# Kernel tuning notes

Measured on AMD Instinct MI355X. Metric: run time of the kernel, lower is better.

The kernel has to match this reference:

```python
import jax, jax.numpy as jnp
import numpy as np

HEADS = 4
OUT_CH = 64
NEG_SLOPE = 0.2  # PyG GATConv default negative_slope


def setup_inputs() -> dict:
    key = jax.random.key(0)
    k1, k2, k3, k4, k5, k6 = jax.random.split(key, 6)
    N, E, IN_CH = 50000, 800000, 128
    x = jax.random.normal(k1, (N, IN_CH), dtype=jnp.float32)
    edge_index = jax.random.randint(k2, (2, E), 0, N, dtype=jnp.int64)
    # Learned parameters (glorot-style init)
    s_w = (6.0 / (IN_CH + HEADS * OUT_CH)) ** 0.5
    W = jax.random.uniform(k3, (IN_CH, HEADS * OUT_CH), minval=-s_w, maxval=s_w, dtype=jnp.float32)
    s_a = (6.0 / (1 + OUT_CH)) ** 0.5
    att_src = jax.random.uniform(k4, (HEADS, OUT_CH), minval=-s_a, maxval=s_a, dtype=jnp.float32)
    att_dst = jax.random.uniform(k5, (HEADS, OUT_CH), minval=-s_a, maxval=s_a, dtype=jnp.float32)
    bias = jnp.zeros((HEADS * OUT_CH,), dtype=jnp.float32)
    return {"x": x, "W": W, "att_src": att_src, "att_dst": att_dst, "bias": bias, "edge_index": edge_index}


def reference(x, W, att_src, att_dst, bias, edge_index):
    # Faithful GATConv (PyG defaults: add_self_loops=True, concat=True, eval mode => no dropout)
    N = x.shape[0]
    loops = jnp.arange(N, dtype=edge_index.dtype)
    src = jnp.concatenate([edge_index[0], loops])  # message source j
    dst = jnp.concatenate([edge_index[1], loops])  # message target i

    xp = (x @ W).reshape(N, HEADS, OUT_CH)          # [N, H, C]
    a_src = jnp.einsum('nhc,hc->nh', xp, att_src)   # [N, H]
    a_dst = jnp.einsum('nhc,hc->nh', xp, att_dst)   # [N, H]

    alpha = jax.nn.leaky_relu(a_src[src] + a_dst[dst], NEG_SLOPE)  # [E', H]
    # segment softmax over incoming edges of each target node
    amax = jax.ops.segment_max(alpha, dst, num_segments=N)
    ex = jnp.exp(alpha - jax.lax.stop_gradient(amax)[dst])
    denom = jax.ops.segment_sum(ex, dst, num_segments=N)
    coef = ex / denom[dst]                           # [E', H]

    msg = xp[src] * coef[:, :, None]                 # [E', H, C]
    out = jax.ops.segment_sum(msg, dst, num_segments=N)  # [N, H, C]
    return out.reshape(N, HEADS * OUT_CH) + bias
```

## Files before the change

### kernel.cpp

```cpp
#include <hip/hip_runtime.h>

#define HEADS 4
#define OUTC 64
#define INC 128
#define HC 256
#define NEG 0.2f

typedef __attribute__((ext_vector_type(8))) short bf16x8;
typedef __attribute__((ext_vector_type(4))) float f32x4;

static __device__ __forceinline__ float bf2f(unsigned short u){
  unsigned int x = ((unsigned int)u) << 16;
  return __uint_as_float(x);
}
static __device__ __forceinline__ unsigned short f2bf(float f){
  unsigned int x = __float_as_uint(f);
  unsigned int lsb = (x >> 16) & 1u;
  x += 0x7fffu + lsb;
  return (unsigned short)(x >> 16);
}
static __device__ __forceinline__ void split8(float4 a, float4 b, bf16x8& hi, bf16x8& lo){
  float v[8] = {a.x, a.y, a.z, a.w, b.x, b.y, b.z, b.w};
  #pragma unroll
  for (int i = 0; i < 8; ++i){
    unsigned short h = f2bf(v[i]);
    hi[i] = (short)h;
    lo[i] = (short)f2bf(v[i] - bf2f(h));
  }
}

#define SPLITB 128

__global__ void k_pre(const float* __restrict__ W, unsigned short* __restrict__ Wthi,
                      unsigned short* __restrict__ Wtlo, const int* __restrict__ ei,
                      int* __restrict__ srcc, int* __restrict__ dstc,
                      int* __restrict__ pos, int* __restrict__ deg, int E){
  if (blockIdx.x < SPLITB){
    int t = blockIdx.x * 256 + threadIdx.x;
    int k = t >> 8, n = t & 255;
    float v = W[t];
    unsigned short hi = f2bf(v);
    Wthi[n * INC + k] = hi;
    Wtlo[n * INC + k] = f2bf(v - bf2f(hi));
    return;
  }
  int e = (blockIdx.x - SPLITB) * 256 + threadIdx.x;
  bool valid = (e < E);
  int ee = valid ? e : 0;
  int hiw = ei[2 * ee + 1];
  bool hz = valid ? (hiw == 0) : true;
  unsigned long long mask = __ballot(hz);
  bool i64 = (mask == ~0ULL);
  int s, d;
  if (i64){ s = ei[2 * ee]; d = ei[2 * (size_t)E + 2 * ee]; }
  else    { s = ei[ee];     d = ei[(size_t)E + ee]; }
  if (valid){
    srcc[e] = s; dstc[e] = d;
    pos[e] = atomicAdd(&deg[d], 1);
  }
}

__global__ __launch_bounds__(256) void k_gemm_scan(const float* __restrict__ X,
    const unsigned short* __restrict__ Wthi, const unsigned short* __restrict__ Wtlo,
    const float* __restrict__ att_src, const float* __restrict__ att_dst,
    unsigned short* __restrict__ XPh, float* __restrict__ a_src, float* __restrict__ a_dst,
    const int* __restrict__ deg, int* __restrict__ rowstart, int* __restrict__ bsum,
    int N, int GB, int nb){
  __shared__ unsigned short shi[64][40];
  __shared__ unsigned short slo[64][40];
  __shared__ int tsum[256];

  if (blockIdx.x >= GB){
    int sb = blockIdx.x - GB;
    int t = threadIdx.x;
    int base = sb * 1024 + t * 4;
    int v[4]; int s = 0;
    #pragma unroll
    for (int k = 0; k < 4; ++k){ int i = base + k; v[k] = (i < N) ? deg[i] : 0; s += v[k]; }
    tsum[t] = s;
    __syncthreads();
    for (int off = 1; off < 256; off <<= 1){
      int x = (t >= off) ? tsum[t - off] : 0;
      __syncthreads();
      tsum[t] += x;
      __syncthreads();
    }
    int excl = tsum[t] - s;
    if (t == 255){
      bsum[sb] = tsum[255];
      if (sb == nb - 1) rowstart[N] = tsum[255];
    }
    int run = excl;
    #pragma unroll
    for (int k = 0; k < 4; ++k){ int i = base + k; if (i < N) rowstart[i] = run; run += v[k]; }
    return;
  }

  int w = threadIdx.x >> 6, lane = threadIdx.x & 63;
  int m0 = blockIdx.x * 64;
  int quad = lane >> 4;
  int l15 = lane & 15;
  int colg[4];
  #pragma unroll
  for (int t = 0; t < 4; ++t) colg[t] = w * 64 + t * 16 + l15;

  bool rv[4];
  #pragma unroll
  for (int rt = 0; rt < 4; ++rt) rv[rt] = (m0 + rt * 16) < N;
  int myrow = rv[w] ? (m0 + w * 16 + l15) : 0;

  f32x4 acc[4][4];
  #pragma unroll
  for (int rt = 0; rt < 4; ++rt)
    #pragma unroll
    for (int t = 0; t < 4; ++t) acc[rt][t] = (f32x4){0.f, 0.f, 0.f, 0.f};

  #pragma unroll
  for (int kk = 0; kk < 4; ++kk){
    const float* xr = X + (size_t)myrow * INC + kk * 32 + quad * 8;
    float4 va = *(const float4*)xr;
    float4 vb = *(const float4*)(xr + 4);
    bf16x8 bh[4], bl[4];
    #pragma unroll
    for (int t = 0; t < 4; ++t){
      size_t bo = (size_t)colg[t] * INC + kk * 32 + quad * 8;
      bh[t] = *(const bf16x8*)(Wthi + bo);
      bl[t] = *(const bf16x8*)(Wtlo + bo);
    }
    bf16x8 ah1, al1;
    split8(va, vb, ah1, al1);
    if (kk) __syncthreads();
    *(bf16x8*)&shi[w * 16 + l15][quad * 8] = ah1;
    *(bf16x8*)&slo[w * 16 + l15][quad * 8] = al1;
    __syncthreads();
    bf16x8 ah[4], al[4];
    #pragma unroll
    for (int rt = 0; rt < 4; ++rt){
      ah[rt] = *(const bf16x8*)&shi[rt * 16 + l15][quad * 8];
      al[rt] = *(const bf16x8*)&slo[rt * 16 + l15][quad * 8];
    }
    #pragma unroll
    for (int rt = 0; rt < 4; ++rt){
      #pragma unroll
      for (int t = 0; t < 4; ++t){
        acc[rt][t] = __builtin_amdgcn_mfma_f32_16x16x32_bf16(ah[rt], bh[t], acc[rt][t], 0, 0, 0);
        acc[rt][t] = __builtin_amdgcn_mfma_f32_16x16x32_bf16(ah[rt], bl[t], acc[rt][t], 0, 0, 0);
        acc[rt][t] = __builtin_amdgcn_mfma_f32_16x16x32_bf16(al[rt], bh[t], acc[rt][t], 0, 0, 0);
      }
    }
  }

  #pragma unroll
  for (int rt = 0; rt < 4; ++rt){
    if (!rv[rt]) continue;
    #pragma unroll
    for (int t = 0; t < 4; ++t){
      #pragma unroll
      for (int r = 0; r < 4; ++r){
        XPh[(size_t)(m0 + rt * 16 + quad * 4 + r) * HC + colg[t]] = f2bf(acc[rt][t][r]);
      }
    }
  }

  float as[4], ad[4];
  #pragma unroll
  for (int t = 0; t < 4; ++t){
    as[t] = att_src[colg[t]];
    ad[t] = att_dst[colg[t]];
  }
  #pragma unroll
  for (int rt = 0; rt < 4; ++rt){
    if (!rv[rt]) continue;
    float ps[4], pd[4];
    #pragma unroll
    for (int r = 0; r < 4; ++r){
      ps[r] = acc[rt][0][r] * as[0] + acc[rt][1][r] * as[1]
            + acc[rt][2][r] * as[2] + acc[rt][3][r] * as[3];
      pd[r] = acc[rt][0][r] * ad[0] + acc[rt][1][r] * ad[1]
            + acc[rt][2][r] * ad[2] + acc[rt][3][r] * ad[3];
    }
    #pragma unroll
    for (int msk = 1; msk < 16; msk <<= 1){
      #pragma unroll
      for (int r = 0; r < 4; ++r){
        ps[r] += __shfl_xor(ps[r], msk, 64);
        pd[r] += __shfl_xor(pd[r], msk, 64);
      }
    }
    if (l15 == 0){
      #pragma unroll
      for (int r = 0; r < 4; ++r){
        int n = m0 + rt * 16 + quad * 4 + r;
        a_src[n * HEADS + w] = ps[r];
        a_dst[n * HEADS + w] = pd[r];
      }
    }
  }
}

__global__ __launch_bounds__(256) void k_scatter(const int* __restrict__ srcc,
                          const int* __restrict__ dstc, const int* __restrict__ pos,
                          const int* __restrict__ rowstart, const int* __restrict__ bsum,
                          int* __restrict__ csr, int E, int nb){
  __shared__ int bps[65];
  int t = threadIdx.x;
  if (t < 64){
    int v = (t < nb) ? bsum[t] : 0;
    #pragma unroll
    for (int off = 1; off < 64; off <<= 1){
      int u = __shfl_up(v, off, 64);
      if (t >= off) v += u;
    }
    bps[t + 1] = v;
    if (t == 0) bps[0] = 0;
  }
  __syncthreads();
  int e = blockIdx.x * 256 + t;
  if (e < E){
    int d = dstc[e];
    csr[rowstart[d] + bps[d >> 10] + pos[e]] = srcc[e];
  }
}

__global__ __launch_bounds__(256) void k_fused(const unsigned short* __restrict__ XPh,
    const float* __restrict__ a_src, const float* __restrict__ a_dst,
    const int* __restrict__ rowstart, const int* __restrict__ bsum,
    const int* __restrict__ csr, const float* __restrict__ bias,
    float* __restrict__ out, int n0, int n1, int nb){
  __shared__ float sh[4][64][4];
  __shared__ int bps[65];
  int w = threadIdx.x >> 6, lane = threadIdx.x & 63;
  if (threadIdx.x < 64){
    int v = (threadIdx.x < nb) ? bsum[threadIdx.x] : 0;
    #pragma unroll
    for (int off = 1; off < 64; off <<= 1){
      int u = __shfl_up(v, off, 64);
      if (threadIdx.x >= off) v += u;
    }
    bps[threadIdx.x + 1] = v;
    if (threadIdx.x == 0) bps[0] = 0;
  }
  __syncthreads();

  int n = n0 + blockIdx.x * 4 + w;
  bool alive = (n < n1);
  if (!alive) n = n0;
  int r0 = rowstart[n] + bps[n >> 10];
  int r1 = rowstart[n + 1] + bps[(n + 1) >> 10];
  int deg = r1 - r0;
  int total = deg + 1;
  int h = lane >> 4;
  float4 ad4 = *(const float4*)&a_dst[n * HEADS];
  bool fast = (total <= 64);
  int jv = n;
  float msel = 0.f, inv_sel = 0.f;

  if (fast){
    if (lane < deg) jv = csr[r0 + lane];
    float l0 = -1e30f, l1 = -1e30f, l2 = -1e30f, l3 = -1e30f;
    if (lane < total){
      float4 a4 = *(const float4*)&a_src[jv * HEADS];
      l0 = a4.x + ad4.x; l0 = (l0 > 0.f) ? l0 : NEG * l0;
      l1 = a4.y + ad4.y; l1 = (l1 > 0.f) ? l1 : NEG * l1;
      l2 = a4.z + ad4.z; l2 = (l2 > 0.f) ? l2 : NEG * l2;
      l3 = a4.w + ad4.w; l3 = (l3 > 0.f) ? l3 : NEG * l3;
    }
    float p0 = __expf(l0), p1 = __expf(l1), p2 = __expf(l2), p3 = __expf(l3);
    float s0 = p0, s1 = p1, s2 = p2, s3 = p3;
    #pragma unroll
    for (int msk = 32; msk; msk >>= 1){
      s0 += __shfl_xor(s0, msk, 64);
      s1 += __shfl_xor(s1, msk, 64);
      s2 += __shfl_xor(s2, msk, 64);
      s3 += __shfl_xor(s3, msk, 64);
    }
    if (lane < total){
      sh[w][lane][0] = p0 / s0;
      sh[w][lane][1] = p1 / s1;
      sh[w][lane][2] = p2 / s2;
      sh[w][lane][3] = p3 / s3;
    }
  } else {
    float m[4] = {-1e30f, -1e30f, -1e30f, -1e30f};
    float s[4] = {0.f, 0.f, 0.f, 0.f};
    float adArr[4] = {ad4.x, ad4.y, ad4.z, ad4.w};
    for (int e = lane; e < total; e += 64){
      int j = (e < deg) ? csr[r0 + e] : n;
      float4 a4 = *(const float4*)&a_src[j * HEADS];
      float aa[4] = {a4.x, a4.y, a4.z, a4.w};
      #pragma unroll
      for (int hh = 0; hh < 4; ++hh){
        float l = aa[hh] + adArr[hh];
        l = (l > 0.f) ? l : NEG * l;
        if (l > m[hh]){ s[hh] = s[hh] * __expf(m[hh] - l) + 1.f; m[hh] = l; }
        else            s[hh] += __expf(l - m[hh]);
      }
    }
    #pragma unroll
    for (int hh = 0; hh < 4; ++hh){
      float mm = m[hh], ss = s[hh];
      #pragma unroll
      for (int msk = 32; msk; msk >>= 1){
        float m2 = __shfl_xor(mm, msk, 64);
        float s2 = __shfl_xor(ss, msk, 64);
        float M = fmaxf(mm, m2);
        float ns = 0.f;
        if (mm > -1e29f) ns += ss * __expf(mm - M);
        if (m2 > -1e29f) ns += s2 * __expf(m2 - M);
        mm = M; ss = ns;
      }
      m[hh] = mm; s[hh] = ss;
    }
    msel    = (h == 0) ? m[0] : (h == 1) ? m[1] : (h == 2) ? m[2] : m[3];
    inv_sel = 1.f / ((h == 0) ? s[0] : (h == 1) ? s[1] : (h == 2) ? s[2] : s[3]);
  }

  float a0 = 0.f, a1 = 0.f, a2 = 0.f, a3 = 0.f;
  const unsigned short* xb = XPh + lane * 4;
  if (fast){
    int e = 0;
    for (; e + 8 <= total; e += 8){
      int jj[8]; float cf[8]; ushort4 xv[8];
      #pragma unroll
      for (int q = 0; q < 8; ++q){
        jj[q] = __builtin_amdgcn_readlane(jv, e + q);
        cf[q] = sh[w][e + q][h];
      }
      #pragma unroll
      for (int q = 0; q < 8; ++q) xv[q] = *(const ushort4*)(xb + (size_t)jj[q] * HC);
      #pragma unroll
      for (int q = 0; q < 8; ++q){
        a0 += cf[q] * bf2f(xv[q].x); a1 += cf[q] * bf2f(xv[q].y);
        a2 += cf[q] * bf2f(xv[q].z); a3 += cf[q] * bf2f(xv[q].w);
      }
    }
    for (; e < total; ++e){
      int j = __builtin_amdgcn_readlane(jv, e);
      float c = sh[w][e][h];
      ushort4 xv = *(const ushort4*)(xb + (size_t)j * HC);
      a0 += c * bf2f(xv.x); a1 += c * bf2f(xv.y); a2 += c * bf2f(xv.z); a3 += c * bf2f(xv.w);
    }
  } else {
    float adh = (h == 0) ? ad4.x : (h == 1) ? ad4.y : (h == 2) ? ad4.z : ad4.w;
    for (int e = 0; e < total; ++e){
      int j = (e < deg) ? csr[r0 + e] : n;
      float4 a4 = *(const float4*)&a_src[j * HEADS];
      float ah = (h == 0) ? a4.x : (h == 1) ? a4.y : (h == 2) ? a4.z : a4.w;
      float l = ah + adh;
      l = (l > 0.f) ? l : NEG * l;
      float c = __expf(l - msel) * inv_sel;
      ushort4 xv = *(const ushort4*)(xb + (size_t)j * HC);
      a0 += c * bf2f(xv.x); a1 += c * bf2f(xv.y); a2 += c * bf2f(xv.z); a3 += c * bf2f(xv.w);
    }
  }
  if (alive){
    float4 b4 = *(const float4*)&bias[lane * 4];
    f32x4 r;
    r[0] = a0 + b4.x; r[1] = a1 + b4.y; r[2] = a2 + b4.z; r[3] = a3 + b4.w;
    __builtin_nontemporal_store(r, (f32x4*)&out[(size_t)n * HC + lane * 4]);
  }
}

extern "C" void kernel_launch(void* const* d_in, const int* in_sizes, int n_in,
                              void* d_out, int out_size, void* d_ws, size_t ws_size,
                              hipStream_t stream){
  const float* x       = (const float*)d_in[0];
  const float* W       = (const float*)d_in[1];
  const float* att_src = (const float*)d_in[2];
  const float* att_dst = (const float*)d_in[3];
  const float* bias    = (const float*)d_in[4];
  const int*   ei      = (const int*)d_in[5];
  int N = in_sizes[0] / INC;
  int E = in_sizes[5] / 2;

  char* p = (char*)d_ws;
  auto alloc = [&](size_t bytes)->char*{
    char* r = p; p += (bytes + 255) & ~(size_t)255; return r;
  };
  unsigned short* Wthi = (unsigned short*)alloc((size_t)INC * HC * 2);
  unsigned short* Wtlo = (unsigned short*)alloc((size_t)INC * HC * 2);
  unsigned short* XPh  = (unsigned short*)alloc((size_t)N * HC * 2);
  float* aSrc          = (float*)alloc((size_t)N * HEADS * 4);
  float* aDst          = (float*)alloc((size_t)N * HEADS * 4);
  int* deg             = (int*)alloc((size_t)N * 4);
  int* rowstart        = (int*)alloc(((size_t)N + 1) * 4);
  int* srcc            = (int*)alloc((size_t)E * 4);
  int* dstc            = (int*)alloc((size_t)E * 4);
  int* pos             = (int*)alloc((size_t)E * 4);
  int* csr             = (int*)alloc((size_t)E * 4);
  int* bsum            = (int*)alloc(256 * 4);

  int GB = (N + 63) / 64;
  int nb = (N + 1023) / 1024;

  hipMemsetAsync(deg, 0, (size_t)N * 4, stream);
  k_pre<<<SPLITB + (E + 255) / 256, 256, 0, stream>>>(W, Wthi, Wtlo, ei,
                                                      srcc, dstc, pos, deg, E);
  k_gemm_scan<<<GB + nb, 256, 0, stream>>>(x, Wthi, Wtlo, att_src, att_dst,
                                           XPh, aSrc, aDst, deg, rowstart, bsum,
                                           N, GB, nb);
  k_scatter<<<(E + 255) / 256, 256, 0, stream>>>(srcc, dstc, pos, rowstart, bsum,
                                                 csr, E, nb);

  int Nh = ((N / 2) + 3) & ~3;
  k_fused<<<(Nh + 3) / 4, 256, 0, stream>>>(XPh, aSrc, aDst, rowstart, bsum, csr,
                                            bias, (float*)d_out, 0, Nh, nb);
  k_fused<<<(N - Nh + 3) / 4, 256, 0, stream>>>(XPh, aSrc, aDst, rowstart, bsum, csr,
                                                bias, (float*)d_out, Nh, N, nb);
}
```

Measured before the change: 242.0 us.

## Merge preprocessing, GEMM and scatter into a persistent kernel with grid barriers

```diff
diff --git a/kernel.cpp b/kernel.cpp
--- a/kernel.cpp
+++ b/kernel.cpp
@@ -30,195 +30,210 @@
 }
 
 #define SPLITB 128
-
-__global__ void k_pre(const float* __restrict__ W, unsigned short* __restrict__ Wthi,
-                      unsigned short* __restrict__ Wtlo, const int* __restrict__ ei,
-                      int* __restrict__ srcc, int* __restrict__ dstc,
-                      int* __restrict__ pos, int* __restrict__ deg, int E){
-  if (blockIdx.x < SPLITB){
-    int t = blockIdx.x * 256 + threadIdx.x;
-    int k = t >> 8, n = t & 255;
-    float v = W[t];
-    unsigned short hi = f2bf(v);
-    Wthi[n * INC + k] = hi;
-    Wtlo[n * INC + k] = f2bf(v - bf2f(hi));
-    return;
-  }
-  int e = (blockIdx.x - SPLITB) * 256 + threadIdx.x;
-  bool valid = (e < E);
-  int ee = valid ? e : 0;
-  int hiw = ei[2 * ee + 1];
-  bool hz = valid ? (hiw == 0) : true;
-  unsigned long long mask = __ballot(hz);
-  bool i64 = (mask == ~0ULL);
-  int s, d;
-  if (i64){ s = ei[2 * ee]; d = ei[2 * (size_t)E + 2 * ee]; }
-  else    { s = ei[ee];     d = ei[(size_t)E + ee]; }
-  if (valid){
-    srcc[e] = s; dstc[e] = d;
-    pos[e] = atomicAdd(&deg[d], 1);
-  }
-}
-
-__global__ __launch_bounds__(256) void k_gemm_scan(const float* __restrict__ X,
-    const unsigned short* __restrict__ Wthi, const unsigned short* __restrict__ Wtlo,
-    const float* __restrict__ att_src, const float* __restrict__ att_dst,
-    unsigned short* __restrict__ XPh, float* __restrict__ a_src, float* __restrict__ a_dst,
-    const int* __restrict__ deg, int* __restrict__ rowstart, int* __restrict__ bsum,
-    int N, int GB, int nb){
+#define GRID 512
+
+static __device__ __forceinline__ void gbar(int* cnt, int target){
+  __syncthreads();
+  if (threadIdx.x == 0){
+    __threadfence();
+    atomicAdd(cnt, 1);
+    while (atomicAdd(cnt, 0) < target){ __builtin_amdgcn_s_sleep(2); }
+  }
+  __syncthreads();
+  __threadfence();
+}
+
+__global__ __launch_bounds__(256, 2) void k_mega(const float* __restrict__ X,
+    const float* __restrict__ W, unsigned short* __restrict__ Wthi,
+    unsigned short* __restrict__ Wtlo, const float* __restrict__ att_src,
+    const float* __restrict__ att_dst, unsigned short* __restrict__ XPh,
+    float* __restrict__ a_src, float* __restrict__ a_dst,
+    const int* __restrict__ ei, int* __restrict__ srcc, int* __restrict__ dstc,
+    int* __restrict__ pos, int* __restrict__ deg, int* __restrict__ rowstart,
+    int* __restrict__ bsum, int* __restrict__ csr, int* __restrict__ cnt,
+    int N, int E, int GB, int EB, int nb){
   __shared__ unsigned short shi[64][40];
   __shared__ unsigned short slo[64][40];
   __shared__ int tsum[256];
-
-  if (blockIdx.x >= GB){
-    int sb = blockIdx.x - GB;
+  __shared__ int bps[65];
+
+  for (int it = blockIdx.x; it < SPLITB + EB; it += GRID){
+    if (it < SPLITB){
+      int t = it * 256 + threadIdx.x;
+      int k = t >> 8, n = t & 255;
+      float v = W[t];
+      unsigned short hi = f2bf(v);
+      Wthi[n * INC + k] = hi;
+      Wtlo[n * INC + k] = f2bf(v - bf2f(hi));
+    } else {
+      int e = (it - SPLITB) * 256 + threadIdx.x;
+      bool valid = (e < E);
+      int ee = valid ? e : 0;
+      int hiw = ei[2 * ee + 1];
+      bool hz = valid ? (hiw == 0) : true;
+      unsigned long long mask = __ballot(hz);
+      bool i64 = (mask == ~0ULL);
+      int s, d;
+      if (i64){ s = ei[2 * ee]; d = ei[2 * (size_t)E + 2 * ee]; }
+      else    { s = ei[ee];     d = ei[(size_t)E + ee]; }
+      if (valid){
+        srcc[e] = s; dstc[e] = d;
+        pos[e] = atomicAdd(&deg[d], 1);
+      }
+    }
+  }
+  gbar(cnt, GRID);
+
+  for (int it = blockIdx.x; it < nb + GB; it += GRID){
+    if (it < nb){
+      int sb = it;
+      int t = threadIdx.x;
+      int base = sb * 1024 + t * 4;
+      int v[4]; int s = 0;
+      #pragma unroll
+      for (int k = 0; k < 4; ++k){ int i = base + k; v[k] = (i < N) ? deg[i] : 0; s += v[k]; }
+      tsum[t] = s;
+      __syncthreads();
+      for (int off = 1; off < 256; off <<= 1){
+        int x = (t >= off) ? tsum[t - off] : 0;
+        __syncthreads();
+        tsum[t] += x;
+        __syncthreads();
+      }
+      int excl = tsum[t] - s;
+      if (t == 255){
+        bsum[sb] = tsum[255];
+        if (sb == nb - 1) rowstart[N] = tsum[255];
+      }
+      int run = excl;
+      #pragma unroll
+      for (int k = 0; k < 4; ++k){ int i = base + k; if (i < N) rowstart[i] = run; run += v[k]; }
+      __syncthreads();
+    } else {
+      int gi = it - nb;
+      int w = threadIdx.x >> 6, lane = threadIdx.x & 63;
+      int m0 = gi * 64;
+      int quad = lane >> 4;
+      int l15 = lane & 15;
+      int colg[4];
+      #pragma unroll
+      for (int t = 0; t < 4; ++t) colg[t] = w * 64 + t * 16 + l15;
+      bool rv[4];
+      #pragma unroll
+      for (int rt = 0; rt < 4; ++rt) rv[rt] = (m0 + rt * 16) < N;
+      int myrow = rv[w] ? (m0 + w * 16 + l15) : 0;
+
+      f32x4 acc[4][4];
+      #pragma unroll
+      for (int rt = 0; rt < 4; ++rt)
+        #pragma unroll
+        for (int t = 0; t < 4; ++t) acc[rt][t] = (f32x4){0.f, 0.f, 0.f, 0.f};
+
+      #pragma unroll
+      for (int kk = 0; kk < 4; ++kk){
+        const float* xr = X + (size_t)myrow * INC + kk * 32 + quad * 8;
+        float4 va = *(const float4*)xr;
+        float4 vb = *(const float4*)(xr + 4);
+        bf16x8 bh[4], bl[4];
+        #pragma unroll
+        for (int t = 0; t < 4; ++t){
+          size_t bo = (size_t)colg[t] * INC + kk * 32 + quad * 8;
+          bh[t] = *(const bf16x8*)(Wthi + bo);
+          bl[t] = *(const bf16x8*)(Wtlo + bo);
+        }
+        bf16x8 ah1, al1;
+        split8(va, vb, ah1, al1);
+        __syncthreads();
+        *(bf16x8*)&shi[w * 16 + l15][quad * 8] = ah1;
+        *(bf16x8*)&slo[w * 16 + l15][quad * 8] = al1;
+        __syncthreads();
+        bf16x8 ah[4], al[4];
+        #pragma unroll
+        for (int rt = 0; rt < 4; ++rt){
+          ah[rt] = *(const bf16x8*)&shi[rt * 16 + l15][quad * 8];
+          al[rt] = *(const bf16x8*)&slo[rt * 16 + l15][quad * 8];
+        }
+        #pragma unroll
+        for (int rt = 0; rt < 4; ++rt){
+          #pragma unroll
+          for (int t = 0; t < 4; ++t){
+            acc[rt][t] = __builtin_amdgcn_mfma_f32_16x16x32_bf16(ah[rt], bh[t], acc[rt][t], 0, 0, 0);
+            acc[rt][t] = __builtin_amdgcn_mfma_f32_16x16x32_bf16(ah[rt], bl[t], acc[rt][t], 0, 0, 0);
+            acc[rt][t] = __builtin_amdgcn_mfma_f32_16x16x32_bf16(al[rt], bh[t], acc[rt][t], 0, 0, 0);
+          }
+        }
+      }
+
+      #pragma unroll
+      for (int rt = 0; rt < 4; ++rt){
+        if (!rv[rt]) continue;
+        #pragma unroll
+        for (int t = 0; t < 4; ++t){
+          #pragma unroll
+          for (int r = 0; r < 4; ++r){
+            XPh[(size_t)(m0 + rt * 16 + quad * 4 + r) * HC + colg[t]] = f2bf(acc[rt][t][r]);
+          }
+        }
+      }
+
+      float as[4], ad[4];
+      #pragma unroll
+      for (int t = 0; t < 4; ++t){
+        as[t] = att_src[colg[t]];
+        ad[t] = att_dst[colg[t]];
+      }
+      #pragma unroll
+      for (int rt = 0; rt < 4; ++rt){
+        if (!rv[rt]) continue;
+        float ps[4], pd[4];
+        #pragma unroll
+        for (int r = 0; r < 4; ++r){
+          ps[r] = acc[rt][0][r] * as[0] + acc[rt][1][r] * as[1]
+                + acc[rt][2][r] * as[2] + acc[rt][3][r] * as[3];
+          pd[r] = acc[rt][0][r] * ad[0] + acc[rt][1][r] * ad[1]
+                + acc[rt][2][r] * ad[2] + acc[rt][3][r] * ad[3];
+        }
+        #pragma unroll
+        for (int msk = 1; msk < 16; msk <<= 1){
+          #pragma unroll
+          for (int r = 0; r < 4; ++r){
+            ps[r] += __shfl_xor(ps[r], msk, 64);
+            pd[r] += __shfl_xor(pd[r], msk, 64);
+          }
+        }
+        if (l15 == 0){
+          #pragma unroll
+          for (int r = 0; r < 4; ++r){
+            int n = m0 + rt * 16 + quad * 4 + r;
+            a_src[n * HEADS + w] = ps[r];
+            a_dst[n * HEADS + w] = pd[r];
+          }
+        }
+      }
+    }
+  }
+  gbar(cnt, 2 * GRID);
+
+  {
     int t = threadIdx.x;
-    int base = sb * 1024 + t * 4;
-    int v[4]; int s = 0;
-    #pragma unroll
-    for (int k = 0; k < 4; ++k){ int i = base + k; v[k] = (i < N) ? deg[i] : 0; s += v[k]; }
-    tsum[t] = s;
+    if (t < 64){
+      int v = (t < nb) ? bsum[t] : 0;
+      #pragma unroll
+      for (int off = 1; off < 64; off <<= 1){
+        int u = __shfl_up(v, off, 64);
+        if (t >= off) v += u;
+      }
+      bps[t + 1] = v;
+      if (t == 0) bps[0] = 0;
+    }
     __syncthreads();
-    for (int off = 1; off < 256; off <<= 1){
-      int x = (t >= off) ? tsum[t - off] : 0;
-      __syncthreads();
-      tsum[t] += x;
-      __syncthreads();
-    }
-    int excl = tsum[t] - s;
-    if (t == 255){
-      bsum[sb] = tsum[255];
-      if (sb == nb - 1) rowstart[N] = tsum[255];
-    }
-    int run = excl;
-    #pragma unroll
-    for (int k = 0; k < 4; ++k){ int i = base + k; if (i < N) rowstart[i] = run; run += v[k]; }
-    return;
-  }
-
-  int w = threadIdx.x >> 6, lane = threadIdx.x & 63;
-  int m0 = blockIdx.x * 64;
-  int quad = lane >> 4;
-  int l15 = lane & 15;
-  int colg[4];
-  #pragma unroll
-  for (int t = 0; t < 4; ++t) colg[t] = w * 64 + t * 16 + l15;
-
-  bool rv[4];
-  #pragma unroll
-  for (int rt = 0; rt < 4; ++rt) rv[rt] = (m0 + rt * 16) < N;
-  int myrow = rv[w] ? (m0 + w * 16 + l15) : 0;
-
-  f32x4 acc[4][4];
-  #pragma unroll
-  for (int rt = 0; rt < 4; ++rt)
-    #pragma unroll
-    for (int t = 0; t < 4; ++t) acc[rt][t] = (f32x4){0.f, 0.f, 0.f, 0.f};
-
-  #pragma unroll
-  for (int kk = 0; kk < 4; ++kk){
-    const float* xr = X + (size_t)myrow * INC + kk * 32 + quad * 8;
-    float4 va = *(const float4*)xr;
-    float4 vb = *(const float4*)(xr + 4);
-    bf16x8 bh[4], bl[4];
-    #pragma unroll
-    for (int t = 0; t < 4; ++t){
-      size_t bo = (size_t)colg[t] * INC + kk * 32 + quad * 8;
-      bh[t] = *(const bf16x8*)(Wthi + bo);
-      bl[t] = *(const bf16x8*)(Wtlo + bo);
-    }
-    bf16x8 ah1, al1;
-    split8(va, vb, ah1, al1);
-    if (kk) __syncthreads();
-    *(bf16x8*)&shi[w * 16 + l15][quad * 8] = ah1;
-    *(bf16x8*)&slo[w * 16 + l15][quad * 8] = al1;
-    __syncthreads();
-    bf16x8 ah[4], al[4];
-    #pragma unroll
-    for (int rt = 0; rt < 4; ++rt){
-      ah[rt] = *(const bf16x8*)&shi[rt * 16 + l15][quad * 8];
-      al[rt] = *(const bf16x8*)&slo[rt * 16 + l15][quad * 8];
-    }
-    #pragma unroll
-    for (int rt = 0; rt < 4; ++rt){
-      #pragma unroll
-      for (int t = 0; t < 4; ++t){
-        acc[rt][t] = __builtin_amdgcn_mfma_f32_16x16x32_bf16(ah[rt], bh[t], acc[rt][t], 0, 0, 0);
-        acc[rt][t] = __builtin_amdgcn_mfma_f32_16x16x32_bf16(ah[rt], bl[t], acc[rt][t], 0, 0, 0);
-        acc[rt][t] = __builtin_amdgcn_mfma_f32_16x16x32_bf16(al[rt], bh[t], acc[rt][t], 0, 0, 0);
-      }
-    }
-  }
-
-  #pragma unroll
-  for (int rt = 0; rt < 4; ++rt){
-    if (!rv[rt]) continue;
-    #pragma unroll
-    for (int t = 0; t < 4; ++t){
-      #pragma unroll
-      for (int r = 0; r < 4; ++r){
-        XPh[(size_t)(m0 + rt * 16 + quad * 4 + r) * HC + colg[t]] = f2bf(acc[rt][t][r]);
-      }
-    }
-  }
-
-  float as[4], ad[4];
-  #pragma unroll
-  for (int t = 0; t < 4; ++t){
-    as[t] = att_src[colg[t]];
-    ad[t] = att_dst[colg[t]];
-  }
-  #pragma unroll
-  for (int rt = 0; rt < 4; ++rt){
-    if (!rv[rt]) continue;
-    float ps[4], pd[4];
-    #pragma unroll
-    for (int r = 0; r < 4; ++r){
-      ps[r] = acc[rt][0][r] * as[0] + acc[rt][1][r] * as[1]
-            + acc[rt][2][r] * as[2] + acc[rt][3][r] * as[3];
-      pd[r] = acc[rt][0][r] * ad[0] + acc[rt][1][r] * ad[1]
-            + acc[rt][2][r] * ad[2] + acc[rt][3][r] * ad[3];
-    }
-    #pragma unroll
-    for (int msk = 1; msk < 16; msk <<= 1){
-      #pragma unroll
-      for (int r = 0; r < 4; ++r){
-        ps[r] += __shfl_xor(ps[r], msk, 64);
-        pd[r] += __shfl_xor(pd[r], msk, 64);
-      }
-    }
-    if (l15 == 0){
-      #pragma unroll
-      for (int r = 0; r < 4; ++r){
-        int n = m0 + rt * 16 + quad * 4 + r;
-        a_src[n * HEADS + w] = ps[r];
-        a_dst[n * HEADS + w] = pd[r];
-      }
-    }
-  }
-}
-
-__global__ __launch_bounds__(256) void k_scatter(const int* __restrict__ srcc,
-                          const int* __restrict__ dstc, const int* __restrict__ pos,
-                          const int* __restrict__ rowstart, const int* __restrict__ bsum,
-                          int* __restrict__ csr, int E, int nb){
-  __shared__ int bps[65];
-  int t = threadIdx.x;
-  if (t < 64){
-    int v = (t < nb) ? bsum[t] : 0;
-    #pragma unroll
-    for (int off = 1; off < 64; off <<= 1){
-      int u = __shfl_up(v, off, 64);
-      if (t >= off) v += u;
-    }
-    bps[t + 1] = v;
-    if (t == 0) bps[0] = 0;
-  }
-  __syncthreads();
-  int e = blockIdx.x * 256 + t;
-  if (e < E){
-    int d = dstc[e];
-    csr[rowstart[d] + bps[d >> 10] + pos[e]] = srcc[e];
+    for (int it = blockIdx.x; it < EB; it += GRID){
+      int e = it * 256 + t;
+      if (e < E){
+        int d = dstc[e];
+        csr[rowstart[d] + bps[d >> 10] + pos[e]] = srcc[e];
+      }
+    }
   }
 }
 
@@ -226,7 +241,7 @@
     const float* __restrict__ a_src, const float* __restrict__ a_dst,
     const int* __restrict__ rowstart, const int* __restrict__ bsum,
     const int* __restrict__ csr, const float* __restrict__ bias,
-    float* __restrict__ out, int n0, int n1, int nb){
+    float* __restrict__ out, int N, int nb){
   __shared__ float sh[4][64][4];
   __shared__ int bps[65];
   int w = threadIdx.x >> 6, lane = threadIdx.x & 63;
@@ -242,9 +257,9 @@
   }
   __syncthreads();
 
-  int n = n0 + blockIdx.x * 4 + w;
-  bool alive = (n < n1);
-  if (!alive) n = n0;
+  int n = blockIdx.x * 4 + w;
+  bool alive = (n < N);
+  if (!alive) n = 0;
   int r0 = rowstart[n] + bps[n >> 10];
   int r1 = rowstart[n + 1] + bps[(n + 1) >> 10];
   int deg = r1 - r0;
@@ -382,6 +397,7 @@
   unsigned short* XPh  = (unsigned short*)alloc((size_t)N * HC * 2);
   float* aSrc          = (float*)alloc((size_t)N * HEADS * 4);
   float* aDst          = (float*)alloc((size_t)N * HEADS * 4);
+  int* cnt             = (int*)alloc(256);
   int* deg             = (int*)alloc((size_t)N * 4);
   int* rowstart        = (int*)alloc(((size_t)N + 1) * 4);
   int* srcc            = (int*)alloc((size_t)E * 4);
@@ -391,20 +407,15 @@
   int* bsum            = (int*)alloc(256 * 4);
 
   int GB = (N + 63) / 64;
+  int EB = (E + 255) / 256;
   int nb = (N + 1023) / 1024;
 
-  hipMemsetAsync(deg, 0, (size_t)N * 4, stream);
-  k_pre<<<SPLITB + (E + 255) / 256, 256, 0, stream>>>(W, Wthi, Wtlo, ei,
-                                                      srcc, dstc, pos, deg, E);
-  k_gemm_scan<<<GB + nb, 256, 0, stream>>>(x, Wthi, Wtlo, att_src, att_dst,
-                                           XPh, aSrc, aDst, deg, rowstart, bsum,
-                                           N, GB, nb);
-  k_scatter<<<(E + 255) / 256, 256, 0, stream>>>(srcc, dstc, pos, rowstart, bsum,
-                                                 csr, E, nb);
-
-  int Nh = ((N / 2) + 3) & ~3;
-  k_fused<<<(Nh + 3) / 4, 256, 0, stream>>>(XPh, aSrc, aDst, rowstart, bsum, csr,
-                                            bias, (float*)d_out, 0, Nh, nb);
-  k_fused<<<(N - Nh + 3) / 4, 256, 0, stream>>>(XPh, aSrc, aDst, rowstart, bsum, csr,
-                                                bias, (float*)d_out, Nh, N, nb);
-}
+  hipMemsetAsync(cnt, 0, 256 + (size_t)N * 4, stream);
+
+  k_mega<<<GRID, 256, 0, stream>>>(x, W, Wthi, Wtlo, att_src, att_dst,
+                                   XPh, aSrc, aDst, ei, srcc, dstc, pos, deg,
+                                   rowstart, bsum, csr, cnt, N, E, GB, EB, nb);
+
+  k_fused<<<(N + 3) / 4, 256, 0, stream>>>(XPh, aSrc, aDst, rowstart, bsum, csr,
+                                           bias, (float*)d_out, N, nb);
+}
```

Measured after the change: 385.1 us. 1.59x slower.
